# Kernel tuning notes

Measured on AMD Instinct MI355X. Metric: run time of the kernel, lower is better.

## Reference

```python
import jax, jax.numpy as jnp
import numpy as np
import heapq
from collections import defaultdict

V = 50257   # vocab_size
D = 512     # embedding_dim
B = 4096    # batch of (embedding, target) samples


def _build_paths(freqs):
    """Huffman tree exactly as in HierarchicalSoftmax.build_tree; returns padded path arrays."""
    heap = [[w, [n]] for n, w in freqs.items()]
    heapq.heapify(heap)
    tree = defaultdict(list)
    while len(heap) > 1:
        lo = heapq.heappop(heap)
        hi = heapq.heappop(heap)
        for node in lo[1]:
            tree[node].append((len(heap), 0))
        for node in hi[1]:
            tree[node].append((len(heap), 1))
        heapq.heappush(heap, [lo[0] + hi[0], lo[1] + hi[1]])
    n_leaves = len(freqs)
    L = max(len(tree[v]) for v in range(n_leaves))  # max path length (~27 for zipf)
    nodes = np.zeros((n_leaves, L), dtype=np.int32)
    dirs = np.zeros((n_leaves, L), dtype=np.int32)
    mask = np.zeros((n_leaves, L), dtype=bool)
    for v in range(n_leaves):
        for i, (p, d) in enumerate(tree[v]):
            nodes[v, i] = p
            dirs[v, i] = d
            mask[v, i] = True
    return nodes, dirs, mask


def setup_inputs() -> dict:
    key = jax.random.key(0)
    k1, k2, k3 = jax.random.split(key, 3)
    freqs = {i: 1.0 / (i + 1) for i in range(V)}  # deterministic zipf frequencies
    nodes, dirs, mask = _build_paths(freqs)
    embeddings = jax.random.normal(k1, (B, D), dtype=jnp.float32)
    # one Linear(D,1) per internal node: V-1 internal nodes total
    W = jax.random.normal(k2, (V - 1, D), dtype=jnp.float32) * (1.0 / np.sqrt(D))
    b = jnp.zeros((V - 1,), dtype=jnp.float32)
    target = jax.random.randint(k3, (B,), 0, V)
    return {
        "embeddings": embeddings,
        "W": W,
        "b": b,
        "target": target,
        "path_nodes": jnp.asarray(nodes),
        "path_dirs": jnp.asarray(dirs),
        "path_mask": jnp.asarray(mask),
    }


def reference(embeddings, W, b, target, path_nodes, path_dirs, path_mask):
    # Gather each sample's root-to-leaf path of internal-node classifiers.
    nodes = path_nodes[target]          # [B, L]
    dirs = path_dirs[target]            # [B, L]
    mask = path_mask[target]            # [B, L] bool
    Wg = W[nodes]                       # [B, L, D] gathered classifier rows
    scores = jnp.einsum('bld,bd->bl', Wg, embeddings) + b[nodes]  # [B, L]
    # direction==1 -> sigmoid(s); direction==0 -> 1 - sigmoid(s) == sigmoid(-s)
    signed = jnp.where(dirs == 1, scores, -scores)
    factors = jnp.where(mask, jax.nn.sigmoid(signed), 1.0)
    return jnp.prod(factors, axis=-1)   # [B] path probabilities
```

## Files before the change

### kernel.cpp

```cpp
#include <hip/hip_runtime.h>


#define HS_D 512

__device__ __forceinline__ float dot8(const float4 e0, const float4 e1,
                                      const float4 a, const float4 b) {
    float p;
    p = e0.x * a.x;
    p = fmaf(e0.y, a.y, p);
    p = fmaf(e0.z, a.z, p);
    p = fmaf(e0.w, a.w, p);
    p = fmaf(e1.x, b.x, p);
    p = fmaf(e1.y, b.y, p);
    p = fmaf(e1.z, b.z, p);
    p = fmaf(e1.w, b.w, p);
    return p;
}

__device__ __forceinline__ float fast_sigmoid(float s) {
    return __builtin_amdgcn_rcpf(1.0f + __expf(-s));
}

__global__ __launch_bounds__(256) void hs_kernel(
    const float* __restrict__ emb,
    const float* __restrict__ W,
    const float* __restrict__ bias,
    const int*   __restrict__ target,
    const int*   __restrict__ nodes,
    const int*   __restrict__ dirs,
    float*       __restrict__ out,
    int B, int L)
{
    const int wid  = blockIdx.x * (blockDim.x >> 6) + (threadIdx.x >> 6);
    const int lane = threadIdx.x & 63;
    if (wid >= B) return;

    const float4* e4 = (const float4*)(emb + (size_t)wid * HS_D);
    const float4 e0 = e4[lane];
    const float4 e1 = e4[lane + 64];

    const int t = __builtin_amdgcn_readfirstlane(target[wid]);

    int nval = 0, dval = 0;
    if (lane < L) {
        nval = nodes[(size_t)t * L + lane];
        dval = dirs [(size_t)t * L + lane];
    }
    const unsigned long long rootmask = __ballot(lane < L && nval == 0);
    const int plen = __ffsll((long long)rootmask);
    const unsigned long long dirmask = __ballot(dval != 0);

    float prod = 1.0f;
    int l = 0;

    for (; l + 4 <= plen; l += 4) {
        const int n0 = __builtin_amdgcn_readfirstlane(__shfl(nval, l + 0, 64));
        const int n1 = __builtin_amdgcn_readfirstlane(__shfl(nval, l + 1, 64));
        const int n2 = __builtin_amdgcn_readfirstlane(__shfl(nval, l + 2, 64));
        const int n3 = __builtin_amdgcn_readfirstlane(__shfl(nval, l + 3, 64));

        const float4* w0 = (const float4*)(W + (size_t)n0 * HS_D);
        const float4* w1 = (const float4*)(W + (size_t)n1 * HS_D);
        const float4* w2 = (const float4*)(W + (size_t)n2 * HS_D);
        const float4* w3 = (const float4*)(W + (size_t)n3 * HS_D);

        const float4 a0 = w0[lane], b0 = w0[lane + 64];
        const float4 a1 = w1[lane], b1 = w1[lane + 64];
        const float4 a2 = w2[lane], b2 = w2[lane + 64];
        const float4 a3 = w3[lane], b3 = w3[lane + 64];

        float p0 = dot8(e0, e1, a0, b0);
        float p1 = dot8(e0, e1, a1, b1);
        float p2 = dot8(e0, e1, a2, b2);
        float p3 = dot8(e0, e1, a3, b3);

        #pragma unroll
        for (int m = 32; m > 0; m >>= 1) {
            p0 += __shfl_xor(p0, m, 64);
            p1 += __shfl_xor(p1, m, 64);
            p2 += __shfl_xor(p2, m, 64);
            p3 += __shfl_xor(p3, m, 64);
        }

        float s0 = p0 + bias[n0];
        float s1 = p1 + bias[n1];
        float s2 = p2 + bias[n2];
        float s3 = p3 + bias[n3];
        s0 = ((dirmask >> (l + 0)) & 1ull) ? s0 : -s0;
        s1 = ((dirmask >> (l + 1)) & 1ull) ? s1 : -s1;
        s2 = ((dirmask >> (l + 2)) & 1ull) ? s2 : -s2;
        s3 = ((dirmask >> (l + 3)) & 1ull) ? s3 : -s3;

        prod *= fast_sigmoid(s0) * fast_sigmoid(s1)
              * fast_sigmoid(s2) * fast_sigmoid(s3);
    }

    for (; l < plen; ++l) {
        const int n = __builtin_amdgcn_readfirstlane(__shfl(nval, l, 64));
        const float4* w = (const float4*)(W + (size_t)n * HS_D);
        const float4 a = w[lane], b = w[lane + 64];
        float p = dot8(e0, e1, a, b);
        #pragma unroll
        for (int m = 32; m > 0; m >>= 1) p += __shfl_xor(p, m, 64);
        float s = p + bias[n];
        s = ((dirmask >> l) & 1ull) ? s : -s;
        prod *= fast_sigmoid(s);
    }

    if (lane == 0) out[wid] = prod;
}

extern "C" void kernel_launch(void* const* d_in, const int* in_sizes, int n_in,
                              void* d_out, int out_size, void* d_ws, size_t ws_size,
                              hipStream_t stream)
{
    const float* emb    = (const float*)d_in[0];
    const float* W      = (const float*)d_in[1];
    const float* bias   = (const float*)d_in[2];
    const int*   target = (const int*)  d_in[3];
    const int*   nodes  = (const int*)  d_in[4];
    const int*   dirs   = (const int*)  d_in[5];
    float*       out    = (float*)d_out;

    const int B = in_sizes[3];
    const int V = in_sizes[2] + 1;
    const int L = in_sizes[4] / V;

    const int wavesPerBlock = 4;
    const int grid = (B + wavesPerBlock - 1) / wavesPerBlock;
    hs_kernel<<<grid, 256, 0, stream>>>(emb, W, bias, target, nodes, dirs, out, B, L);
}
```

Baseline: 163.9 us.

## Split each sample's path across a block with 16-lane groups per node

Each block now handles a single sample. Its 4 waves are split into 16-lane groups, and each group computes the dot product for a different path node, so up to 16 path nodes are processed concurrently instead of serially in steps of 4. Each lane loads 8 float4s of the embedding and W row, and the shuffle reduction shrinks to 4 steps. Per-group factors are combined with cross-lane and shared-memory products. This exposes more memory-level parallelism and shortens the serial dependency chain per sample, at the cost of 4x more blocks, redundant embedding loads per wave, and a __syncthreads.

```diff
diff --git a/kernel.cpp b/kernel.cpp
--- a/kernel.cpp
+++ b/kernel.cpp
@@ -2,23 +2,23 @@
 
 
 #define HS_D 512
-
-__device__ __forceinline__ float dot8(const float4 e0, const float4 e1,
-                                      const float4 a, const float4 b) {
-    float p;
-    p = e0.x * a.x;
-    p = fmaf(e0.y, a.y, p);
-    p = fmaf(e0.z, a.z, p);
-    p = fmaf(e0.w, a.w, p);
-    p = fmaf(e1.x, b.x, p);
-    p = fmaf(e1.y, b.y, p);
-    p = fmaf(e1.z, b.z, p);
-    p = fmaf(e1.w, b.w, p);
-    return p;
-}
+#define F4PL 8
 
 __device__ __forceinline__ float fast_sigmoid(float s) {
     return __builtin_amdgcn_rcpf(1.0f + __expf(-s));
+}
+
+__device__ __forceinline__ float dot32(const float4* __restrict__ e,
+                                       const float4* __restrict__ a) {
+    float p = e[0].x * a[0].x;
+    #pragma unroll
+    for (int k = 0; k < F4PL; ++k) {
+        if (k) p = fmaf(e[k].x, a[k].x, p);
+        p = fmaf(e[k].y, a[k].y, p);
+        p = fmaf(e[k].z, a[k].z, p);
+        p = fmaf(e[k].w, a[k].w, p);
+    }
+    return p;
 }
 
 __global__ __launch_bounds__(256) void hs_kernel(
@@ -31,15 +31,15 @@
     float*       __restrict__ out,
     int B, int L)
 {
-    const int wid  = blockIdx.x * (blockDim.x >> 6) + (threadIdx.x >> 6);
+    const int b    = blockIdx.x;
+    const int wv   = threadIdx.x >> 6;
     const int lane = threadIdx.x & 63;
-    if (wid >= B) return;
+    const int g    = lane >> 4;
+    const int gl   = lane & 15;
 
-    const float4* e4 = (const float4*)(emb + (size_t)wid * HS_D);
-    const float4 e0 = e4[lane];
-    const float4 e1 = e4[lane + 64];
+    __shared__ float wprod[4];
 
-    const int t = __builtin_amdgcn_readfirstlane(target[wid]);
+    const int t = __builtin_amdgcn_readfirstlane(target[b]);
 
     int nval = 0, dval = 0;
     if (lane < L) {
@@ -50,64 +50,76 @@
     const int plen = __ffsll((long long)rootmask);
     const unsigned long long dirmask = __ballot(dval != 0);
 
-    float prod = 1.0f;
-    int l = 0;
+    const float4* e4 = (const float4*)(emb + (size_t)b * HS_D);
+    float4 ek[F4PL];
+    #pragma unroll
+    for (int k = 0; k < F4PL; ++k) ek[k] = e4[gl + 16 * k];
 
-    for (; l + 4 <= plen; l += 4) {
-        const int n0 = __builtin_amdgcn_readfirstlane(__shfl(nval, l + 0, 64));
-        const int n1 = __builtin_amdgcn_readfirstlane(__shfl(nval, l + 1, 64));
-        const int n2 = __builtin_amdgcn_readfirstlane(__shfl(nval, l + 2, 64));
-        const int n3 = __builtin_amdgcn_readfirstlane(__shfl(nval, l + 3, 64));
+    const int l0 = wv + 4 * g;
+    const int l1 = l0 + 16;
+    const int n0 = __shfl(nval, l0, 64);
+    const int n1 = __shfl(nval, l1, 64);
+    const bool act0 = (l0 < plen);
+    const bool act1 = (l1 < plen);
 
-        const float4* w0 = (const float4*)(W + (size_t)n0 * HS_D);
-        const float4* w1 = (const float4*)(W + (size_t)n1 * HS_D);
-        const float4* w2 = (const float4*)(W + (size_t)n2 * HS_D);
-        const float4* w3 = (const float4*)(W + (size_t)n3 * HS_D);
+    float lprod = 1.0f;
 
-        const float4 a0 = w0[lane], b0 = w0[lane + 64];
-        const float4 a1 = w1[lane], b1 = w1[lane + 64];
-        const float4 a2 = w2[lane], b2 = w2[lane + 64];
-        const float4 a3 = w3[lane], b3 = w3[lane + 64];
-
-        float p0 = dot8(e0, e1, a0, b0);
-        float p1 = dot8(e0, e1, a1, b1);
-        float p2 = dot8(e0, e1, a2, b2);
-        float p3 = dot8(e0, e1, a3, b3);
-
+    float4 a1[F4PL];
+    if (act1) {
+        const float4* w4 = (const float4*)(W + (size_t)n1 * HS_D);
         #pragma unroll
-        for (int m = 32; m > 0; m >>= 1) {
-            p0 += __shfl_xor(p0, m, 64);
-            p1 += __shfl_xor(p1, m, 64);
-            p2 += __shfl_xor(p2, m, 64);
-            p3 += __shfl_xor(p3, m, 64);
-        }
-
-        float s0 = p0 + bias[n0];
-        float s1 = p1 + bias[n1];
-        float s2 = p2 + bias[n2];
-        float s3 = p3 + bias[n3];
-        s0 = ((dirmask >> (l + 0)) & 1ull) ? s0 : -s0;
-        s1 = ((dirmask >> (l + 1)) & 1ull) ? s1 : -s1;
-        s2 = ((dirmask >> (l + 2)) & 1ull) ? s2 : -s2;
-        s3 = ((dirmask >> (l + 3)) & 1ull) ? s3 : -s3;
-
-        prod *= fast_sigmoid(s0) * fast_sigmoid(s1)
-              * fast_sigmoid(s2) * fast_sigmoid(s3);
+        for (int k = 0; k < F4PL; ++k) a1[k] = w4[gl + 16 * k];
     }
 
-    for (; l < plen; ++l) {
-        const int n = __builtin_amdgcn_readfirstlane(__shfl(nval, l, 64));
-        const float4* w = (const float4*)(W + (size_t)n * HS_D);
-        const float4 a = w[lane], b = w[lane + 64];
-        float p = dot8(e0, e1, a, b);
+    if (act0) {
+        const float4* w4 = (const float4*)(W + (size_t)n0 * HS_D);
+        float4 a0[F4PL];
         #pragma unroll
-        for (int m = 32; m > 0; m >>= 1) p += __shfl_xor(p, m, 64);
-        float s = p + bias[n];
-        s = ((dirmask >> l) & 1ull) ? s : -s;
-        prod *= fast_sigmoid(s);
+        for (int k = 0; k < F4PL; ++k) a0[k] = w4[gl + 16 * k];
+        const float bi = bias[n0];
+        float p = dot32(ek, a0);
+        #pragma unroll
+        for (int m = 8; m >= 1; m >>= 1) p += __shfl_xor(p, m, 64);
+        float s = p + bi;
+        s = ((dirmask >> l0) & 1ull) ? s : -s;
+        lprod = fast_sigmoid(s);
     }
 
-    if (lane == 0) out[wid] = prod;
+    if (act1) {
+        const float bi = bias[n1];
+        float p = dot32(ek, a1);
+        #pragma unroll
+        for (int m = 8; m >= 1; m >>= 1) p += __shfl_xor(p, m, 64);
+        float s = p + bi;
+        s = ((dirmask >> l1) & 1ull) ? s : -s;
+        lprod *= fast_sigmoid(s);
+    }
+
+    for (int base = wv + 32; base < plen; base += 16) {
+        const int l  = base + 4 * g;
+        const int ls = (l < 64) ? l : 0;
+        const int n  = __shfl(nval, ls, 64);
+        if (l < plen) {
+            const float4* w4 = (const float4*)(W + (size_t)n * HS_D);
+            float4 a[F4PL];
+            #pragma unroll
+            for (int k = 0; k < F4PL; ++k) a[k] = w4[gl + 16 * k];
+            float p = dot32(ek, a);
+            #pragma unroll
+            for (int m = 8; m >= 1; m >>= 1) p += __shfl_xor(p, m, 64);
+            float s = p + bias[n];
+            s = ((dirmask >> l) & 1ull) ? s : -s;
+            lprod *= fast_sigmoid(s);
+        }
+    }
+
+    lprod *= __shfl_xor(lprod, 16, 64);
+    lprod *= __shfl_xor(lprod, 32, 64);
+
+    if (lane == 0) wprod[wv] = lprod;
+    __syncthreads();
+    if (threadIdx.x == 0)
+        out[b] = wprod[0] * wprod[1] * wprod[2] * wprod[3];
 }
 
 extern "C" void kernel_launch(void* const* d_in, const int* in_sizes, int n_in,
@@ -126,7 +138,5 @@
     const int V = in_sizes[2] + 1;
     const int L = in_sizes[4] / V;
 
-    const int wavesPerBlock = 4;
-    const int grid = (B + wavesPerBlock - 1) / wavesPerBlock;
-    hs_kernel<<<grid, 256, 0, stream>>>(emb, W, bias, target, nodes, dirs, out, B, L);
+    hs_kernel<<<B, 256, 0, stream>>>(emb, W, bias, target, nodes, dirs, out, B, L);
 }
```

Measured after the change: 168.5 us. 2.8% more time.
